# Optimization experiments

Hardware: AMD Instinct MI355X
Metric: run time of the kernel (lower is better)

Reference implementation:

```python
import jax, jax.numpy as jnp
import numpy as np

H = 32        # num query heads
KVH = 8       # num kv heads
HD = 64       # head dim
G = H // KVH  # GQA group size
THETA = 10000.0


def _rope(x, pos):
    # x: [B, h, S, HD], pos: [B, S] int
    inv_freq = 1.0 / (THETA ** (jnp.arange(0, HD, 2, dtype=jnp.float32) / HD))  # [HD/2]
    freqs = pos.astype(jnp.float32)[:, :, None] * inv_freq[None, None, :]        # [B, S, HD/2]
    emb = jnp.concatenate([freqs, freqs], axis=-1)                               # [B, S, HD]
    cos = jnp.cos(emb)[:, None, :, :].astype(x.dtype)                            # [B, 1, S, HD]
    sin = jnp.sin(emb)[:, None, :, :].astype(x.dtype)
    x1, x2 = x[..., : HD // 2], x[..., HD // 2 :]
    rot = jnp.concatenate([-x2, x1], axis=-1)
    return x * cos + rot * sin


def setup_inputs() -> dict:
    key = jax.random.key(0)
    ks = jax.random.split(key, 8)
    B, S, D = 2, 2048, 2048
    s = 0.02
    hidden_states = jax.random.normal(ks[0], (B, S, D), dtype=jnp.float32)
    position_ids = jnp.broadcast_to(jnp.arange(S, dtype=jnp.int32)[None, :], (B, S))
    Wq = jax.random.normal(ks[1], (H * HD, D), dtype=jnp.float32) * s
    bq = jax.random.normal(ks[2], (H * HD,), dtype=jnp.float32) * s
    Wk = jax.random.normal(ks[3], (KVH * HD, D), dtype=jnp.float32) * s
    bk = jax.random.normal(ks[4], (KVH * HD,), dtype=jnp.float32) * s
    Wv = jax.random.normal(ks[5], (KVH * HD, D), dtype=jnp.float32) * s
    bv = jax.random.normal(ks[6], (KVH * HD,), dtype=jnp.float32) * s
    Wo = jax.random.normal(ks[7], (D, H * HD), dtype=jnp.float32) * s
    return dict(hidden_states=hidden_states, position_ids=position_ids,
                Wq=Wq, bq=bq, Wk=Wk, bk=bk, Wv=Wv, bv=bv, Wo=Wo)


def reference(hidden_states, position_ids, Wq, bq, Wk, bk, Wv, bv, Wo):
    B, S, D = hidden_states.shape
    scale = 1.0 / np.sqrt(HD)
    q = hidden_states @ Wq.T + bq  # [B, S, H*HD]
    k = hidden_states @ Wk.T + bk  # [B, S, KVH*HD]
    v = hidden_states @ Wv.T + bv
    q = q.reshape(B, S, H, HD).transpose(0, 2, 1, 3)      # [B, H, S, HD]
    k = k.reshape(B, S, KVH, HD).transpose(0, 2, 1, 3)    # [B, KVH, S, HD]
    v = v.reshape(B, S, KVH, HD).transpose(0, 2, 1, 3)
    q = _rope(q, position_ids)
    k = _rope(k, position_ids)
    # GQA: view q as [B, KVH, G, S, HD]; equivalent math to repeat_kv of k/v
    qg = q.reshape(B, KVH, G, S, HD)
    scores = jnp.einsum('bkgqd,bkld->bkgql', qg, k) * scale  # [B, KVH, G, S, S]
    # causal mask (past_seq_len = 0)
    causal = jnp.tril(jnp.ones((S, S), dtype=bool))
    scores = jnp.where(causal[None, None, None, :, :], scores, jnp.float32(-jnp.inf))
    attn = jax.nn.softmax(scores.astype(jnp.float32), axis=-1).astype(q.dtype)
    out = jnp.einsum('bkgql,bkld->bkgqd', attn, v)            # [B, KVH, G, S, HD]
    out = out.reshape(B, H, S, HD).transpose(0, 2, 1, 3).reshape(B, S, H * HD)
    return out @ Wo.T
```

## Files before the change

### kernel.cpp

```cpp
#include <hip/hip_runtime.h>
#include <hip/hip_bf16.h>

typedef unsigned short u16;
typedef __bf16 bf16x8 __attribute__((ext_vector_type(8)));
typedef float f32x4 __attribute__((ext_vector_type(4)));
typedef float f32x4v __attribute__((ext_vector_type(4)));
typedef unsigned short u16x4 __attribute__((ext_vector_type(4)));

__device__ __forceinline__ u16 f2bf(float f) {
  __bf16 h = (__bf16)f;
  return __builtin_bit_cast(unsigned short, h);
}

__device__ __forceinline__ int permh(int ph) {
  int blk = ph >> 4;
  int pblk = (blk == 1) ? 2 : ((blk == 2) ? 1 : blk);
  return (pblk << 4) | (ph & 15);
}

__device__ __forceinline__ int SW(int r, int c) {
  return (r << 6) + (c ^ ((r & 7) << 3));
}

#define GLOAD_LDS16(gp, lp) __builtin_amdgcn_global_load_lds( \
    (const __attribute__((address_space(1))) unsigned int*)(gp), \
    (__attribute__((address_space(3))) unsigned int*)(lp), 16, 0, 0)

#define BAR() do { asm volatile("" ::: "memory"); __builtin_amdgcn_s_barrier(); asm volatile("" ::: "memory"); } while (0)
#define VMCNT(n) asm volatile("s_waitcnt vmcnt(" #n ")" ::: "memory")

__global__ void prep_all(const f32x4v* __restrict__ hs, u16x4* __restrict__ hsb,
                         const f32x4v* __restrict__ wq, const f32x4v* __restrict__ wk,
                         const f32x4v* __restrict__ wv, u16x4* __restrict__ wqkvb,
                         const f32x4v* __restrict__ wo, u16x4* __restrict__ wob,
                         const int* __restrict__ pos, float* __restrict__ cosT,
                         float* __restrict__ sinT, const float* __restrict__ bq,
                         const float* __restrict__ bk, const float* __restrict__ bv,
                         float* __restrict__ bc) {
  int i = blockIdx.x * 256 + threadIdx.x;
  if (i < 2097152) {
    f32x4v v = hs[i];
    u16x4 o; o.x = f2bf(v.x); o.y = f2bf(v.y); o.z = f2bf(v.z); o.w = f2bf(v.w);
    hsb[i] = o;
  } else if (i < 3670016) {
    int j = i - 2097152;
    int row = j >> 9, c4 = j & 511;
    f32x4v v;
    if (row < 2048) {
      int sr = (row & ~63) | permh(row & 63);
      v = wq[(size_t)sr * 512 + c4];
    } else if (row < 2560) {
      int rk = row - 2048;
      int sr = (rk & ~63) | permh(rk & 63);
      v = wk[(size_t)sr * 512 + c4];
    } else {
      v = wv[(size_t)(row - 2560) * 512 + c4];
    }
    u16x4 o; o.x = f2bf(v.x); o.y = f2bf(v.y); o.z = f2bf(v.z); o.w = f2bf(v.w);
    wqkvb[j] = o;
  } else if (i < 4718592) {
    int j = i - 3670016;
    f32x4v v = wo[j];
    u16x4 o; o.x = f2bf(v.x); o.y = f2bf(v.y); o.z = f2bf(v.z); o.w = f2bf(v.w);
    wob[j] = o;
  } else if (i < 4849664) {
    int j = i - 4718592;
    int bs = j >> 5, f = j & 31;
    float inv = exp2f(-(float)f * (13.287712379549449f / 32.f));
    float ang = (float)pos[bs] * inv;
    cosT[j] = cosf(ang);
    sinT[j] = sinf(ang);
  } else if (i < 4852736) {
    int j = i - 4849664;
    float v;
    if (j < 2048) {
      v = bq[(j & ~63) | permh(j & 63)];
    } else if (j < 2560) {
      int jk = j - 2048;
      v = bk[(jk & ~63) | permh(jk & 63)];
    } else {
      v = bv[j - 2560];
    }
    bc[j] = v;
  }
}

#define STAGE8(op, kt, hh) { \
    const u16* s_ = ((op) ? bS : aS) + (size_t)(hh) * 128 * K + (size_t)(kt) * 64; \
    u16* d_ = lds + ((kt) & 1) * 32768 + (op) * 16384 + (hh) * 8192 + wid * 512; \
    GLOAD_LDS16(s_, d_); \
    GLOAD_LDS16(s_ + (size_t)64 * K, d_ + 4096); \
  }

#define LDA8(buf, qm) { \
    const u16* p_ = lds + (buf) * 32768 + ((qm) * 128 + arow) * 64; \
    _Pragma("unroll") \
    for (int mf = 0; mf < 4; ++mf) { \
      af[mf][0] = *(const bf16x8*)(p_ + mf * 1024 + koff0); \
      af[mf][1] = *(const bf16x8*)(p_ + mf * 1024 + koff1); \
    } }

#define LDB8(buf, qn) { \
    const u16* p_ = lds + (buf) * 32768 + 16384 + ((qn) * 128 + brow) * 64; \
    _Pragma("unroll") \
    for (int nf = 0; nf < 2; ++nf) { \
      bfr[nf][0] = *(const bf16x8*)(p_ + nf * 1024 + koff0); \
      bfr[nf][1] = *(const bf16x8*)(p_ + nf * 1024 + koff1); \
    } }

#define MM8(qm, qn) { \
    __builtin_amdgcn_s_setprio(1); \
    _Pragma("unroll") \
    for (int mf = 0; mf < 4; ++mf) \
      _Pragma("unroll") \
      for (int nf = 0; nf < 2; ++nf) { \
        acc[(qm) * 4 + mf][(qn) * 2 + nf] = __builtin_amdgcn_mfma_f32_16x16x32_bf16( \
            af[mf][0], bfr[nf][0], acc[(qm) * 4 + mf][(qn) * 2 + nf], 0, 0, 0); \
        acc[(qm) * 4 + mf][(qn) * 2 + nf] = __builtin_amdgcn_mfma_f32_16x16x32_bf16( \
            af[mf][1], bfr[nf][1], acc[(qm) * 4 + mf][(qn) * 2 + nf], 0, 0, 0); \
      } \
    __builtin_amdgcn_s_setprio(0); }

template <int MODE>
__global__ __launch_bounds__(512, 2) void gemm8(
    const u16* __restrict__ A, const u16* __restrict__ Bw, const int K, const int N,
    u16* __restrict__ qb, u16* __restrict__ kb, u16* __restrict__ vtb,
    const float* __restrict__ biasc, const float* __restrict__ cosT,
    const float* __restrict__ sinT, float* __restrict__ outf) {
  __shared__ u16 lds[65536];
  const int tid = threadIdx.x;
  const int lane = tid & 63, wid = tid >> 6;
  const int wr = wid >> 2, wc = wid & 3;
  const int col = lane & 15, rg = lane >> 4;
  const int tm = blockIdx.x, tn = blockIdx.y;

  const int srow = tid >> 3;
  const int scol = ((tid & 7) ^ (srow & 7)) * 8;
  const u16* aS = A + ((size_t)tm * 256 + srow) * K + scol;
  const u16* bS = Bw + ((size_t)tn * 256 + srow) * K + scol;

  const int koff0 = (rg ^ (col & 7)) * 8;
  const int koff1 = ((4 + rg) ^ (col & 7)) * 8;
  const int arow = wr * 64 + col;
  const int brow = wc * 32 + col;

  f32x4 acc[8][4];
#pragma unroll
  for (int i = 0; i < 8; ++i)
#pragma unroll
    for (int j = 0; j < 4; ++j) acc[i][j] = (f32x4){0.f, 0.f, 0.f, 0.f};
  bf16x8 af[4][2], bfr[2][2];

  const int ITERS = K >> 7;

  STAGE8(0, 0, 0); STAGE8(0, 0, 1);
  STAGE8(1, 0, 0); STAGE8(1, 0, 1);
  STAGE8(0, 1, 0); STAGE8(1, 1, 1); STAGE8(0, 1, 1);
  VMCNT(6);
  BAR();

#pragma unroll 1
  for (int it = 0; it < ITERS; ++it) {
    const int t0 = it * 2;
    const bool more = (it + 1 < ITERS);
    LDA8(0, 0); LDB8(0, 0);
    STAGE8(1, t0 + 1, 0);
    BAR(); MM8(0, 0); BAR();
    LDB8(0, 1);
    if (more) STAGE8(0, t0 + 2, 0);
    BAR(); MM8(0, 1); BAR();
    LDA8(0, 1);
    if (more) STAGE8(1, t0 + 2, 1);
    BAR(); MM8(1, 1); BAR();
    LDB8(0, 0);
    if (more) STAGE8(0, t0 + 2, 1);
    BAR(); MM8(1, 0);
    if (more) { VMCNT(6); } else { VMCNT(0); }
    BAR();
    LDA8(1, 0); LDB8(1, 0);
    if (more) STAGE8(1, t0 + 2, 0);
    BAR(); MM8(0, 0); BAR();
    LDB8(1, 1);
    if (more) STAGE8(0, t0 + 3, 0);
    BAR(); MM8(0, 1); BAR();
    LDA8(1, 1);
    if (more) STAGE8(1, t0 + 3, 1);
    BAR(); MM8(1, 1); BAR();
    LDB8(1, 0);
    if (more) STAGE8(0, t0 + 3, 1);
    BAR(); MM8(1, 0);
    if (more) VMCNT(6);
    BAR();
  }

  if (MODE == 1) {
#pragma unroll
    for (int qm = 0; qm < 2; ++qm)
#pragma unroll
      for (int mf = 0; mf < 4; ++mf) {
        const int mbase = tm * 256 + qm * 128 + wr * 64 + mf * 16 + rg * 4;
#pragma unroll
        for (int qn = 0; qn < 2; ++qn)
#pragma unroll
          for (int nf = 0; nf < 2; ++nf) {
            const int n = tn * 256 + qn * 128 + wc * 32 + nf * 16 + col;
#pragma unroll
            for (int r = 0; r < 4; ++r)
              outf[(size_t)(mbase + r) * N + n] = acc[qm * 4 + mf][qn * 2 + nf][r];
          }
      }
  } else {
    if (tn < 8) {
      const float QS = 0.18033688011112042f;
#pragma unroll
      for (int qm = 0; qm < 2; ++qm)
#pragma unroll
        for (int qn = 0; qn < 2; ++qn) {
          const int h = tn * 4 + qn * 2 + (wc >> 1);
          const int c32 = wc & 1;
          const int n0 = tn * 256 + qn * 128 + wc * 32 + col;
          const float b1 = biasc[n0], b2 = biasc[n0 + 16];
          const int f = c32 * 16 + col;
          const int ph0 = c32 * 32 + col;
#pragma unroll
          for (int mf = 0; mf < 4; ++mf)
#pragma unroll
            for (int r = 0; r < 4; ++r) {
              const int m = tm * 256 + qm * 128 + wr * 64 + mf * 16 + rg * 4 + r;
              const int b = m >> 11, s = m & 2047;
              const size_t base = ((size_t)(b * 32 + h) * 2048 + s) * 64;
              float x1 = acc[qm * 4 + mf][qn * 2 + 0][r] + b1;
              float x2 = acc[qm * 4 + mf][qn * 2 + 1][r] + b2;
              float c = cosT[m * 32 + f], sn = sinT[m * 32 + f];
              qb[base + ph0]      = f2bf((x1 * c - x2 * sn) * QS);
              qb[base + ph0 + 16] = f2bf((x2 * c + x1 * sn) * QS);
            }
        }
    } else if (tn < 10) {
#pragma unroll
      for (int qm = 0; qm < 2; ++qm)
#pragma unroll
        for (int qn = 0; qn < 2; ++qn) {
          const int hk = (tn - 8) * 4 + qn * 2 + (wc >> 1);
          const int c32 = wc & 1;
          const int n0 = tn * 256 + qn * 128 + wc * 32 + col;
          const float b1 = biasc[n0], b2 = biasc[n0 + 16];
          const int f = c32 * 16 + col;
          const int ph0 = c32 * 32 + col;
#pragma unroll
          for (int mf = 0; mf < 4; ++mf)
#pragma unroll
            for (int r = 0; r < 4; ++r) {
              const int m = tm * 256 + qm * 128 + wr * 64 + mf * 16 + rg * 4 + r;
              const int b = m >> 11, s = m & 2047;
              const size_t base = ((size_t)(b * 8 + hk) * 2048 + s) * 64;
              float x1 = acc[qm * 4 + mf][qn * 2 + 0][r] + b1;
              float x2 = acc[qm * 4 + mf][qn * 2 + 1][r] + b2;
              float c = cosT[m * 32 + f], sn = sinT[m * 32 + f];
              kb[base + ph0]      = f2bf(x1 * c - x2 * sn);
              kb[base + ph0 + 16] = f2bf(x2 * c + x1 * sn);
            }
        }
    } else {
#pragma unroll
      for (int qm = 0; qm < 2; ++qm)
#pragma unroll
        for (int qn = 0; qn < 2; ++qn)
#pragma unroll
          for (int nf = 0; nf < 2; ++nf) {
            const int n = tn * 256 + qn * 128 + wc * 32 + nf * 16 + col;
            const int hk = (n - 2560) >> 6;
            const int d = (n - 2560) & 63;
            const float bvv = biasc[n];
#pragma unroll
            for (int mf = 0; mf < 4; ++mf)
#pragma unroll
              for (int r = 0; r < 4; ++r) {
                const int m = tm * 256 + qm * 128 + wr * 64 + mf * 16 + rg * 4 + r;
                const int b = m >> 11, s = m & 2047;
                vtb[((size_t)(b * 8 + hk) * 64 + d) * 2048 + s] =
                    f2bf(acc[qm * 4 + mf][qn * 2 + nf][r] + bvv);
              }
          }
    }
  }
}

__global__ __launch_bounds__(256, 4) void attn_k(
    const u16* __restrict__ qb, const u16* __restrict__ kb,
    const u16* __restrict__ vtb, u16* __restrict__ attb) {
  __shared__ __align__(16) u16 Kl[2][2048];
  __shared__ __align__(16) u16 Vl[2][2048];
  __shared__ __align__(16) u16 Pl[4096];
  const int tid = threadIdx.x, lane = tid & 63, w = tid >> 6;
  const int col = lane & 15, rg = lane >> 4;

  const int bid = blockIdx.x;
  const int xcd = bid & 7, pos = bid >> 3;
  const int grp = xcd * 8 + (pos >> 4);
  const int s0 = pos & 15;
  const int strip = ((pos >> 5) & 1) ? (15 - s0) : s0;
  const int h = grp & 31, b = grp >> 5;
  const int qb0 = (15 - strip) * 128;
  const int hk = h >> 2;
  const int q0w = qb0 + w * 32;

  const u16* Qp = qb + ((size_t)(b * 32 + h) * 2048 + q0w + col) * 64 + rg * 8;
  bf16x8 qf[2][2];
#pragma unroll
  for (int g = 0; g < 2; ++g)
#pragma unroll
    for (int kf = 0; kf < 2; ++kf)
      qf[g][kf] = *(const bf16x8*)(Qp + g * 16 * 64 + kf * 32);

  f32x4 po[2][4];
  float l_part[2] = {0.f, 0.f};
#pragma unroll
  for (int g = 0; g < 2; ++g)
#pragma unroll
    for (int cf = 0; cf < 4; ++cf) po[g][cf] = (f32x4){0, 0, 0, 0};

  const u16* Kbase = kb + (size_t)(b * 8 + hk) * 2048 * 64;
  const u16* Vbase = vtb + (size_t)(b * 8 + hk) * 64 * 2048;
  const int srow = tid >> 3, c8 = (tid & 7) << 3;
  const int cs = c8 ^ ((srow & 7) << 3);
  const u16* Ksrc = Kbase + (size_t)srow * 64 + cs;
  const u16* Vsrc = Vbase + (size_t)(srow * 2 + (cs >> 5)) * 2048 + (cs & 31);
  char* Kdst0 = (char*)Kl + w * 1024;
  char* Vdst0 = (char*)Vl + w * 1024;

  const int nkv = (qb0 >> 5) + 4;
  const int rowmax = q0w + 31;

  GLOAD_LDS16(Ksrc, Kdst0);
  GLOAD_LDS16(Vsrc, Vdst0);
  __syncthreads();

  for (int it = 0; it < nkv; ++it) {
    const int kv0 = it * 32;
    const int buf = it & 1;
    if (it + 1 < nkv) {
      GLOAD_LDS16(Ksrc + (size_t)(it + 1) * 2048, Kdst0 + ((it + 1) & 1) * 4096);
      GLOAD_LDS16(Vsrc + (size_t)(it + 1) * 32, Vdst0 + ((it + 1) & 1) * 4096);
    }

    if (kv0 <= rowmax) {
      const u16* Kb = (const u16*)((const char*)Kl + buf * 4096);
      const u16* Vb = (const u16*)((const char*)Vl + buf * 4096);
      const bool diag = (kv0 + 32 > q0w);

#pragma unroll
      for (int cj = 0; cj < 2; ++cj) {
        const int krow = cj * 16 + col;
        bf16x8 k0f = *(const bf16x8*)&Kb[SW(krow, rg * 8)];
        bf16x8 k1f = *(const bf16x8*)&Kb[SW(krow, 32 + rg * 8)];
#pragma unroll
        for (int g = 0; g < 2; ++g) {
          f32x4 t = (f32x4){0, 0, 0, 0};
          t = __builtin_amdgcn_mfma_f32_16x16x32_bf16(k0f, qf[g][0], t, 0, 0, 0);
          t = __builtin_amdgcn_mfma_f32_16x16x32_bf16(k1f, qf[g][1], t, 0, 0, 0);
          const int q = q0w + g * 16 + col;
          if (diag) {
            const int kbase = kv0 + cj * 16 + rg * 4;
#pragma unroll
            for (int r = 0; r < 4; ++r)
              if (kbase + r > q) t[r] = -1e30f;
          }
          float p0 = __builtin_amdgcn_exp2f(t[0]);
          float p1 = __builtin_amdgcn_exp2f(t[1]);
          float p2 = __builtin_amdgcn_exp2f(t[2]);
          float p3 = __builtin_amdgcn_exp2f(t[3]);
          l_part[g] += (p0 + p1) + (p2 + p3);
          unsigned w0, w1;
          asm("v_cvt_pk_bf16_f32 %0, %1, %2" : "=v"(w0) : "v"(p0), "v"(p1));
          asm("v_cvt_pk_bf16_f32 %0, %1, %2" : "=v"(w1) : "v"(p2), "v"(p3));
          const int lq = w * 32 + g * 16 + col;
          const int prow = lq >> 1;
          const int pc = ((lq & 1) * 32 + cj * 16 + rg * 4) ^ ((prow & 7) << 3);
          *(uint2*)&Pl[prow * 64 + pc] = (uint2){w0, w1};
        }
      }

      __builtin_amdgcn_s_setprio(1);
      {
        bf16x8 pfr[2];
#pragma unroll
        for (int g = 0; g < 2; ++g) {
          const int lq = w * 32 + g * 16 + col;
          const int prow = lq >> 1;
          pfr[g] = *(const bf16x8*)&Pl[prow * 64 +
                     (((lq & 1) * 32 + rg * 8) ^ ((prow & 7) << 3))];
        }
#pragma unroll
        for (int cf = 0; cf < 4; ++cf) {
          const int d = cf * 16 + col;
          const int vrow = d >> 1;
          bf16x8 vf = *(const bf16x8*)&Vb[vrow * 64 +
                       (((d & 1) * 32 + rg * 8) ^ ((vrow & 7) << 3))];
          po[0][cf] = __builtin_amdgcn_mfma_f32_16x16x32_bf16(pfr[0], vf, po[0][cf], 0, 0, 0);
          po[1][cf] = __builtin_amdgcn_mfma_f32_16x16x32_bf16(pfr[1], vf, po[1][cf], 0, 0, 0);
        }
      }
      __builtin_amdgcn_s_setprio(0);
    }
    __syncthreads();
  }

#pragma unroll
  for (int g = 0; g < 2; ++g) {
    float l = l_part[g];
    l += __shfl_xor(l, 16);
    l += __shfl_xor(l, 32);
    l_part[g] = l;
  }
#pragma unroll
  for (int g = 0; g < 2; ++g)
#pragma unroll
    for (int r = 0; r < 4; ++r) {
      const float lq = __shfl(l_part[g], rg * 4 + r, 16);
      const float inv = 1.f / lq;
      const int qrow = q0w + g * 16 + rg * 4 + r;
      size_t base = ((size_t)b * 2048 + qrow) * 2048 + h * 64;
#pragma unroll
      for (int cf = 0; cf < 4; ++cf)
        attb[base + cf * 16 + col] = f2bf(po[g][cf][r] * inv);
    }
}

extern "C" void kernel_launch(void* const* d_in, const int* in_sizes, int n_in,
                              void* d_out, int out_size, void* d_ws, size_t ws_size,
                              hipStream_t stream) {
  const float* hs = (const float*)d_in[0];
  const int* pos = (const int*)d_in[1];
  const float* Wq = (const float*)d_in[2];
  const float* bq = (const float*)d_in[3];
  const float* Wk = (const float*)d_in[4];
  const float* bk = (const float*)d_in[5];
  const float* Wv = (const float*)d_in[6];
  const float* bv = (const float*)d_in[7];
  const float* Wo = (const float*)d_in[8];
  float* out = (float*)d_out;

  char* ws = (char*)d_ws;
  size_t off = 0;
  u16* hsb = (u16*)(ws + off);   off += (size_t)4096 * 2048 * 2;
  u16* wqkvb = (u16*)(ws + off); off += (size_t)3072 * 2048 * 2;
  u16* wob = (u16*)(ws + off);   off += (size_t)2048 * 2048 * 2;
  float* biasc = (float*)(ws + off); off += 3072 * 4;
  float* cosT = (float*)(ws + off);  off += (size_t)4096 * 32 * 4;
  float* sinT = (float*)(ws + off);  off += (size_t)4096 * 32 * 4;
  u16* qb = (u16*)(ws + off);    off += (size_t)2 * 32 * 2048 * 64 * 2;
  u16* kb = (u16*)(ws + off);    off += (size_t)2 * 8 * 2048 * 64 * 2;
  u16* vtb = (u16*)(ws + off);   off += (size_t)2 * 8 * 64 * 2048 * 2;
  u16* attb = (u16*)(ws + off);  off += (size_t)4096 * 2048 * 2;

  prep_all<<<18956, 256, 0, stream>>>((const f32x4v*)hs, (u16x4*)hsb,
                                      (const f32x4v*)Wq, (const f32x4v*)Wk,
                                      (const f32x4v*)Wv, (u16x4*)wqkvb,
                                      (const f32x4v*)Wo, (u16x4*)wob,
                                      pos, cosT, sinT, bq, bk, bv, biasc);

  gemm8<0><<<dim3(16, 12), 512, 0, stream>>>(hsb, wqkvb, 2048, 3072,
                                             qb, kb, vtb, biasc, cosT, sinT, nullptr);
  attn_k<<<1024, 256, 0, stream>>>(qb, kb, vtb, attb);
  gemm8<1><<<dim3(16, 8), 512, 0, stream>>>(attb, wob, 2048, 2048,
                                            nullptr, nullptr, nullptr, nullptr,
                                            nullptr, nullptr, out);
}
```

Measured before the change: 200.9 us.

## Template GEMM on M-tile size; use 128-row tiles for output projection

Measured after the change: 176.6 us. -12.1%, faster.

```diff
diff --git a/kernel.cpp b/kernel.cpp
--- a/kernel.cpp
+++ b/kernel.cpp
@@ -28,6 +28,7 @@
 
 #define BAR() do { asm volatile("" ::: "memory"); __builtin_amdgcn_s_barrier(); asm volatile("" ::: "memory"); } while (0)
 #define VMCNT(n) asm volatile("s_waitcnt vmcnt(" #n ")" ::: "memory")
+#define SBAR0() __builtin_amdgcn_sched_barrier(0)
 
 __global__ void prep_all(const f32x4v* __restrict__ hs, u16x4* __restrict__ hsb,
                          const f32x4v* __restrict__ wq, const f32x4v* __restrict__ wk,
@@ -85,23 +86,30 @@
   }
 }
 
-#define STAGE8(op, kt, hh) { \
-    const u16* s_ = ((op) ? bS : aS) + (size_t)(hh) * 128 * K + (size_t)(kt) * 64; \
-    u16* d_ = lds + ((kt) & 1) * 32768 + (op) * 16384 + (hh) * 8192 + wid * 512; \
+#define STAGE_A(kt, hh) { \
+    const u16* s_ = aS + (size_t)(hh) * (BM / 2) * K + (size_t)(kt) * 64; \
+    u16* d_ = lds + ((kt) & 1) * BUF + (hh) * (BM * 32) + wid * 512; \
+    GLOAD_LDS16(s_, d_); \
+    if constexpr (BM == 256) GLOAD_LDS16(s_ + (size_t)64 * K, d_ + 4096); \
+  }
+
+#define STAGE_B(kt, hh) { \
+    const u16* s_ = bS + (size_t)(hh) * 128 * K + (size_t)(kt) * 64; \
+    u16* d_ = lds + ((kt) & 1) * BUF + BM * 64 + (hh) * 8192 + wid * 512; \
     GLOAD_LDS16(s_, d_); \
     GLOAD_LDS16(s_ + (size_t)64 * K, d_ + 4096); \
   }
 
 #define LDA8(buf, qm) { \
-    const u16* p_ = lds + (buf) * 32768 + ((qm) * 128 + arow) * 64; \
+    const u16* p_ = lds + (buf) * BUF + ((qm) * (BM / 2) + arow) * 64; \
     _Pragma("unroll") \
-    for (int mf = 0; mf < 4; ++mf) { \
+    for (int mf = 0; mf < MF; ++mf) { \
       af[mf][0] = *(const bf16x8*)(p_ + mf * 1024 + koff0); \
       af[mf][1] = *(const bf16x8*)(p_ + mf * 1024 + koff1); \
     } }
 
 #define LDB8(buf, qn) { \
-    const u16* p_ = lds + (buf) * 32768 + 16384 + ((qn) * 128 + brow) * 64; \
+    const u16* p_ = lds + (buf) * BUF + BM * 64 + ((qn) * 128 + brow) * 64; \
     _Pragma("unroll") \
     for (int nf = 0; nf < 2; ++nf) { \
       bfr[nf][0] = *(const bf16x8*)(p_ + nf * 1024 + koff0); \
@@ -111,23 +119,27 @@
 #define MM8(qm, qn) { \
     __builtin_amdgcn_s_setprio(1); \
     _Pragma("unroll") \
-    for (int mf = 0; mf < 4; ++mf) \
+    for (int mf = 0; mf < MF; ++mf) \
       _Pragma("unroll") \
       for (int nf = 0; nf < 2; ++nf) { \
-        acc[(qm) * 4 + mf][(qn) * 2 + nf] = __builtin_amdgcn_mfma_f32_16x16x32_bf16( \
-            af[mf][0], bfr[nf][0], acc[(qm) * 4 + mf][(qn) * 2 + nf], 0, 0, 0); \
-        acc[(qm) * 4 + mf][(qn) * 2 + nf] = __builtin_amdgcn_mfma_f32_16x16x32_bf16( \
-            af[mf][1], bfr[nf][1], acc[(qm) * 4 + mf][(qn) * 2 + nf], 0, 0, 0); \
+        acc[(qm) * MF + mf][(qn) * 2 + nf] = __builtin_amdgcn_mfma_f32_16x16x32_bf16( \
+            af[mf][0], bfr[nf][0], acc[(qm) * MF + mf][(qn) * 2 + nf], 0, 0, 0); \
+        acc[(qm) * MF + mf][(qn) * 2 + nf] = __builtin_amdgcn_mfma_f32_16x16x32_bf16( \
+            af[mf][1], bfr[nf][1], acc[(qm) * MF + mf][(qn) * 2 + nf], 0, 0, 0); \
       } \
     __builtin_amdgcn_s_setprio(0); }
 
-template <int MODE>
+#define VMCNT_GATE() do { if constexpr (BM == 256) { VMCNT(6); } else { VMCNT(4); } } while (0)
+
+template <int MODE, int BM>
 __global__ __launch_bounds__(512, 2) void gemm8(
     const u16* __restrict__ A, const u16* __restrict__ Bw, const int K, const int N,
     u16* __restrict__ qb, u16* __restrict__ kb, u16* __restrict__ vtb,
     const float* __restrict__ biasc, const float* __restrict__ cosT,
     const float* __restrict__ sinT, float* __restrict__ outf) {
-  __shared__ u16 lds[65536];
+  constexpr int MF = BM / 64;
+  constexpr int BUF = BM * 64 + 16384;
+  __shared__ u16 lds[2 * BUF];
   const int tid = threadIdx.x;
   const int lane = tid & 63, wid = tid >> 6;
   const int wr = wid >> 2, wc = wid & 3;
@@ -136,27 +148,27 @@
 
   const int srow = tid >> 3;
   const int scol = ((tid & 7) ^ (srow & 7)) * 8;
-  const u16* aS = A + ((size_t)tm * 256 + srow) * K + scol;
+  const u16* aS = A + ((size_t)tm * BM + srow) * K + scol;
   const u16* bS = Bw + ((size_t)tn * 256 + srow) * K + scol;
 
   const int koff0 = (rg ^ (col & 7)) * 8;
   const int koff1 = ((4 + rg) ^ (col & 7)) * 8;
-  const int arow = wr * 64 + col;
+  const int arow = wr * (BM / 4) + col;
   const int brow = wc * 32 + col;
 
-  f32x4 acc[8][4];
-#pragma unroll
-  for (int i = 0; i < 8; ++i)
+  f32x4 acc[2 * MF][4];
+#pragma unroll
+  for (int i = 0; i < 2 * MF; ++i)
 #pragma unroll
     for (int j = 0; j < 4; ++j) acc[i][j] = (f32x4){0.f, 0.f, 0.f, 0.f};
-  bf16x8 af[4][2], bfr[2][2];
+  bf16x8 af[MF][2], bfr[2][2];
 
   const int ITERS = K >> 7;
 
-  STAGE8(0, 0, 0); STAGE8(0, 0, 1);
-  STAGE8(1, 0, 0); STAGE8(1, 0, 1);
-  STAGE8(0, 1, 0); STAGE8(1, 1, 1); STAGE8(0, 1, 1);
-  VMCNT(6);
+  STAGE_A(0, 0); STAGE_A(0, 1);
+  STAGE_B(0, 0); STAGE_B(0, 1);
+  STAGE_A(1, 0); STAGE_B(1, 1); STAGE_A(1, 1);
+  VMCNT_GATE();
   BAR();
 
 #pragma unroll 1
@@ -164,41 +176,41 @@
     const int t0 = it * 2;
     const bool more = (it + 1 < ITERS);
     LDA8(0, 0); LDB8(0, 0);
-    STAGE8(1, t0 + 1, 0);
-    BAR(); MM8(0, 0); BAR();
+    STAGE_B(t0 + 1, 0);
+    MM8(0, 0); SBAR0(); BAR();
     LDB8(0, 1);
-    if (more) STAGE8(0, t0 + 2, 0);
-    BAR(); MM8(0, 1); BAR();
+    if (more) STAGE_A(t0 + 2, 0);
+    MM8(0, 1); SBAR0(); BAR();
     LDA8(0, 1);
-    if (more) STAGE8(1, t0 + 2, 1);
-    BAR(); MM8(1, 1); BAR();
+    if (more) STAGE_B(t0 + 2, 1);
+    MM8(1, 1); SBAR0(); BAR();
     LDB8(0, 0);
-    if (more) STAGE8(0, t0 + 2, 1);
-    BAR(); MM8(1, 0);
-    if (more) { VMCNT(6); } else { VMCNT(0); }
+    if (more) STAGE_A(t0 + 2, 1);
+    MM8(1, 0); SBAR0();
+    if (more) { VMCNT_GATE(); } else { VMCNT(0); }
     BAR();
     LDA8(1, 0); LDB8(1, 0);
-    if (more) STAGE8(1, t0 + 2, 0);
-    BAR(); MM8(0, 0); BAR();
+    if (more) STAGE_B(t0 + 2, 0);
+    MM8(0, 0); SBAR0(); BAR();
     LDB8(1, 1);
-    if (more) STAGE8(0, t0 + 3, 0);
-    BAR(); MM8(0, 1); BAR();
+    if (more) STAGE_A(t0 + 3, 0);
+    MM8(0, 1); SBAR0(); BAR();
     LDA8(1, 1);
-    if (more) STAGE8(1, t0 + 3, 1);
-    BAR(); MM8(1, 1); BAR();
+    if (more) STAGE_B(t0 + 3, 1);
+    MM8(1, 1); SBAR0(); BAR();
     LDB8(1, 0);
-    if (more) STAGE8(0, t0 + 3, 1);
-    BAR(); MM8(1, 0);
-    if (more) VMCNT(6);
+    if (more) STAGE_A(t0 + 3, 1);
+    MM8(1, 0); SBAR0();
+    if (more) VMCNT_GATE();
     BAR();
   }
 
-  if (MODE == 1) {
+  if constexpr (MODE == 1) {
 #pragma unroll
     for (int qm = 0; qm < 2; ++qm)
 #pragma unroll
-      for (int mf = 0; mf < 4; ++mf) {
-        const int mbase = tm * 256 + qm * 128 + wr * 64 + mf * 16 + rg * 4;
+      for (int mf = 0; mf < MF; ++mf) {
+        const int mbase = tm * BM + qm * (BM / 2) + wr * (BM / 4) + mf * 16 + rg * 4;
 #pragma unroll
         for (int qn = 0; qn < 2; ++qn)
 #pragma unroll
@@ -206,7 +218,7 @@
             const int n = tn * 256 + qn * 128 + wc * 32 + nf * 16 + col;
 #pragma unroll
             for (int r = 0; r < 4; ++r)
-              outf[(size_t)(mbase + r) * N + n] = acc[qm * 4 + mf][qn * 2 + nf][r];
+              outf[(size_t)(mbase + r) * N + n] = acc[qm * MF + mf][qn * 2 + nf][r];
           }
       }
   } else {
@@ -223,14 +235,14 @@
           const int f = c32 * 16 + col;
           const int ph0 = c32 * 32 + col;
 #pragma unroll
-          for (int mf = 0; mf < 4; ++mf)
+          for (int mf = 0; mf < MF; ++mf)
 #pragma unroll
             for (int r = 0; r < 4; ++r) {
               const int m = tm * 256 + qm * 128 + wr * 64 + mf * 16 + rg * 4 + r;
               const int b = m >> 11, s = m & 2047;
               const size_t base = ((size_t)(b * 32 + h) * 2048 + s) * 64;
-              float x1 = acc[qm * 4 + mf][qn * 2 + 0][r] + b1;
-              float x2 = acc[qm * 4 + mf][qn * 2 + 1][r] + b2;
+              float x1 = acc[qm * MF + mf][qn * 2 + 0][r] + b1;
+              float x2 = acc[qm * MF + mf][qn * 2 + 1][r] + b2;
               float c = cosT[m * 32 + f], sn = sinT[m * 32 + f];
               qb[base + ph0]      = f2bf((x1 * c - x2 * sn) * QS);
               qb[base + ph0 + 16] = f2bf((x2 * c + x1 * sn) * QS);
@@ -248,14 +260,14 @@
           const int f = c32 * 16 + col;
           const int ph0 = c32 * 32 + col;
 #pragma unroll
-          for (int mf = 0; mf < 4; ++mf)
+          for (int mf = 0; mf < MF; ++mf)
 #pragma unroll
             for (int r = 0; r < 4; ++r) {
               const int m = tm * 256 + qm * 128 + wr * 64 + mf * 16 + rg * 4 + r;
               const int b = m >> 11, s = m & 2047;
               const size_t base = ((size_t)(b * 8 + hk) * 2048 + s) * 64;
-              float x1 = acc[qm * 4 + mf][qn * 2 + 0][r] + b1;
-              float x2 = acc[qm * 4 + mf][qn * 2 + 1][r] + b2;
+              float x1 = acc[qm * MF + mf][qn * 2 + 0][r] + b1;
+              float x2 = acc[qm * MF + mf][qn * 2 + 1][r] + b2;
               float c = cosT[m * 32 + f], sn = sinT[m * 32 + f];
               kb[base + ph0]      = f2bf(x1 * c - x2 * sn);
               kb[base + ph0 + 16] = f2bf(x2 * c + x1 * sn);
@@ -273,13 +285,13 @@
             const int d = (n - 2560) & 63;
             const float bvv = biasc[n];
 #pragma unroll
-            for (int mf = 0; mf < 4; ++mf)
+            for (int mf = 0; mf < MF; ++mf)
 #pragma unroll
               for (int r = 0; r < 4; ++r) {
                 const int m = tm * 256 + qm * 128 + wr * 64 + mf * 16 + rg * 4 + r;
                 const int b = m >> 11, s = m & 2047;
                 vtb[((size_t)(b * 8 + hk) * 64 + d) * 2048 + s] =
-                    f2bf(acc[qm * 4 + mf][qn * 2 + nf][r] + bvv);
+                    f2bf(acc[qm * MF + mf][qn * 2 + nf][r] + bvv);
               }
           }
     }
@@ -460,10 +472,10 @@
                                       (const f32x4v*)Wo, (u16x4*)wob,
                                       pos, cosT, sinT, bq, bk, bv, biasc);
 
-  gemm8<0><<<dim3(16, 12), 512, 0, stream>>>(hsb, wqkvb, 2048, 3072,
-                                             qb, kb, vtb, biasc, cosT, sinT, nullptr);
+  gemm8<0, 256><<<dim3(16, 12), 512, 0, stream>>>(hsb, wqkvb, 2048, 3072,
+                                                  qb, kb, vtb, biasc, cosT, sinT, nullptr);
   attn_k<<<1024, 256, 0, stream>>>(qb, kb, vtb, attb);
-  gemm8<1><<<dim3(16, 8), 512, 0, stream>>>(attb, wob, 2048, 2048,
-                                            nullptr, nullptr, nullptr, nullptr,
-                                            nullptr, nullptr, out);
-}
+  gemm8<1, 128><<<dim3(32, 8), 512, 0, stream>>>(attb, wob, 2048, 2048,
+                                                 nullptr, nullptr, nullptr, nullptr,
+                                                 nullptr, nullptr, out);
+}
```
